# Kernel optimization log

Measured on AMD Instinct MI355X. Metric: run time of the kernel, lower is better.

Reference implementation:

```python
import jax, jax.numpy as jnp
import numpy as np

G = 128          # resolution
NE = 4           # n_emotions
SIGMA = 0.05     # splat kernel width
ETA = 0.01       # global write strength
ALPHA_H = 0.002
ALPHA_E = 0.001
LEAK = 5e-05
RADIUS = max(2, int(3.0 * SIGMA * G / 2.0))   # = 9
W = 2 * RADIUS + 1                            # = 19


def _laplacian(x):
    # 6-neighbor Laplacian with replicate padding; x: [..., G, G, G]
    pad = [(0, 0)] * (x.ndim - 3) + [(1, 1)] * 3
    p = jnp.pad(x, pad, mode='edge')
    c = p[..., 1:-1, 1:-1, 1:-1]
    return (p[..., :-2, 1:-1, 1:-1] + p[..., 2:, 1:-1, 1:-1]
            + p[..., 1:-1, :-2, 1:-1] + p[..., 1:-1, 2:, 1:-1]
            + p[..., 1:-1, 1:-1, :-2] + p[..., 1:-1, 1:-1, 2:]
            - 6.0 * c)


def _splat(H, E, positions, intensities, emotions):
    # Gaussian splat scatter-add into H [G,G,G] and E [NE,G,G,G].
    gp = (positions + 1.0) * 0.5 * (G - 1)                       # [N,3] grid coords
    c = jnp.clip(jnp.floor(gp).astype(jnp.int32), 0, G - 1)      # center cell
    offs = jnp.arange(-RADIUS, RADIUS + 1, dtype=jnp.int32)
    coords = c[:, :, None] + offs[None, None, :]                 # [N,3,W]
    valid = (coords >= 0) & (coords < G)
    cc = jnp.clip(coords, 0, G - 1)
    sig = SIGMA * G / 2.0
    d = coords.astype(gp.dtype) - gp[:, :, None]                 # [N,3,W]
    k1 = jnp.where(valid, jnp.exp(-(d * d) / (2.0 * sig * sig)), 0.0)
    kx, ky, kz = k1[:, 0], k1[:, 1], k1[:, 2]                    # [N,W] each (separable)
    omega = intensities * ETA                                    # [N]
    vals = (omega[:, None, None, None] * kx[:, :, None, None]
            * ky[:, None, :, None] * kz[:, None, None, :])       # [N,W,W,W]
    flat = ((cc[:, 0][:, :, None, None] * G + cc[:, 1][:, None, :, None]) * G
            + cc[:, 2][:, None, None, :]).reshape(-1)            # [N*W^3]
    H_new = H.reshape(-1).at[flat].add(vals.reshape(-1)).reshape(G, G, G)
    E_ch = []
    for e in range(NE):
        ve = (vals * emotions[:, e][:, None, None, None]).reshape(-1)
        E_ch.append(E[e].reshape(-1).at[flat].add(ve).reshape(G, G, G))
    return H_new, jnp.stack(E_ch)


def _step(H, E):
    H2 = jnp.maximum(H * (1.0 - LEAK) + ALPHA_H * _laplacian(H), 0.0)
    E2 = jnp.maximum(E * (1.0 - LEAK) + LEAK + ALPHA_E * _laplacian(E), 0.0)
    return H2, E2


def _sample(H, E, sp):
    # grid_sample trilinear, padding_mode='border', align_corners=True.
    # grid_sample axis convention: sp[...,0]->last axis, sp[...,1]->middle, sp[...,2]->first.
    B, T, _ = sp.shape
    t = jnp.clip((sp.reshape(-1, 3) + 1.0) * 0.5 * (G - 1), 0.0, G - 1)  # [BT,3]
    i0 = jnp.floor(t).astype(jnp.int32)
    f = t - i0
    i0 = jnp.clip(i0, 0, G - 1)
    i1 = jnp.clip(i0 + 1, 0, G - 1)
    x0, y0, z0 = i0[:, 0], i0[:, 1], i0[:, 2]
    x1, y1, z1 = i1[:, 0], i1[:, 1], i1[:, 2]
    fx, fy, fz = f[:, 0], f[:, 1], f[:, 2]

    def interp(vol):  # vol [..., G,G,G] -> [..., BT]
        out = 0.0
        for zi, wz in ((z0, 1.0 - fz), (z1, fz)):
            for yi, wy in ((y0, 1.0 - fy), (y1, fy)):
                for xi, wx in ((x0, 1.0 - fx), (x1, fx)):
                    out = out + vol[..., zi, yi, xi] * (wz * wy * wx)
        return out

    p_H = interp(H).reshape(B, T)
    p_E = interp(E).T.reshape(B, T, NE)
    return p_H, p_E


def setup_inputs() -> dict:
    key = jax.random.key(0)
    k1, k2, k3, k4 = jax.random.split(key, 4)
    N, B, T = 4096, 8, 1024
    return {
        'positions': jax.random.uniform(k1, (N, 3), jnp.float32, -0.95, 0.95),
        'intensities': jax.random.uniform(k2, (N,), jnp.float32),
        'emotions': jax.random.uniform(k3, (N, NE), jnp.float32),
        'sample_positions': jax.random.uniform(k4, (B, T, 3), jnp.float32, -1.0, 1.0),
        'H0': jnp.zeros((G, G, G), jnp.float32),
        'E0': jnp.ones((NE, G, G, G), jnp.float32),
    }


def reference(positions, intensities, emotions, sample_positions, H0, E0):
    H, E = _splat(H0, E0, positions, intensities, emotions)
    H, E = _step(H, E)
    p_H, p_E = _sample(H, E, sample_positions)
    return jnp.concatenate([p_H[..., None], p_E], axis=-1)  # [B,T,1+NE]
```

## Files before the change

### kernel.cpp

```cpp
#include <hip/hip_runtime.h>


namespace {
constexpr int   G      = 128;
constexpr int   G3     = G * G * G;
constexpr int   NE     = 4;
constexpr int   RAD    = 9;
constexpr float SIG    = 0.05f * (float)G * 0.5f;
constexpr float INV2S2 = 1.0f / (2.0f * SIG * SIG);
constexpr float ETA    = 0.01f;
constexpr float A_H    = 0.002f;
constexpr float A_E    = 0.001f;
constexpr float LEAK   = 5e-5f;

constexpr int T0 = 4, T1 = 4, T2 = 32;
constexpr int NT0 = G / T0, NT1 = G / T1, NT2 = G / T2;
constexpr int NTILES = NT0 * NT1 * NT2;
constexpr int CAP = 96;
}

__device__ __forceinline__ int clampi(int v, int lo, int hi) {
    return min(max(v, lo), hi);
}

__global__ void __launch_bounds__(256) bin_meta_kernel(
        const float* __restrict__ pos, const float* __restrict__ inten,
        const float4* __restrict__ emo4,
        int* __restrict__ counts, int* __restrict__ lists,
        float4* __restrict__ meta, int N) {
    const int p    = blockIdx.x * 4 + (threadIdx.x >> 6);
    const int lane = threadIdx.x & 63;
    if (p >= N) return;

    const float gx = (pos[p * 3 + 0] + 1.0f) * 0.5f * (float)(G - 1);
    const float gy = (pos[p * 3 + 1] + 1.0f) * 0.5f * (float)(G - 1);
    const float gz = (pos[p * 3 + 2] + 1.0f) * 0.5f * (float)(G - 1);
    const int c0 = clampi((int)floorf(gx), 0, G - 1);
    const int c1 = clampi((int)floorf(gy), 0, G - 1);
    const int c2 = clampi((int)floorf(gz), 0, G - 1);

    if (lane == 0) {
        meta[2 * p]     = make_float4(gx, gy, gz, inten[p] * ETA);
        meta[2 * p + 1] = emo4[p];
    }

    const int l0 = max(c0 - RAD, 0) >> 2, h0 = min(c0 + RAD, G - 1) >> 2;
    const int l1 = max(c1 - RAD, 0) >> 2, h1 = min(c1 + RAD, G - 1) >> 2;
    const int l2 = max(c2 - RAD, 0) >> 5, h2 = min(c2 + RAD, G - 1) >> 5;
    const int n0 = h0 - l0, n1 = h1 - l1, n2 = h2 - l2;

    for (int s = lane; s < 72; s += 64) {
        const int a = s / 12;
        const int r = s - a * 12;
        const int b = r >> 1;
        const int cs = r & 1;
        if (a <= n0 && b <= n1 && cs <= n2) {
            const int t = ((l0 + a) * NT1 + (l1 + b)) * NT2 + (l2 + cs);
            const int slot = atomicAdd(&counts[t], 1);
            if (slot < CAP) lists[t * CAP + slot] = p;
        }
    }
}

__global__ void __launch_bounds__(256) gather_kernel(
        const float4* __restrict__ meta,
        const float* __restrict__ H0, const float* __restrict__ E0,
        const int* __restrict__ counts, const int* __restrict__ lists,
        float* __restrict__ ws) {
    const int tile = blockIdx.x;
    const int t2 = tile % NT2, t1 = (tile / NT2) % NT1, t0 = tile / (NT2 * NT1);
    const int tid = threadIdx.x;

    __shared__ float kx[CAP * 4];
    __shared__ float ky[CAP * 4];
    __shared__ float kz[CAP * 32];

    const int cnt = min(counts[tile], CAP);
    const int* __restrict__ lst = lists + tile * CAP;

    const int b0 = t0 * T0, b1 = t1 * T1, b2 = t2 * T2;
    for (int t = tid; t < cnt * 40; t += 256) {
        const int n = t / 40;
        const int s = t - n * 40;
        const int p = lst[n];
        const int axis = (s < 4) ? 0 : (s < 8) ? 1 : 2;
        const int off  = (s < 4) ? s : (s < 8) ? s - 4 : s - 8;
        const float4 mg = meta[2 * p];
        const float g = (axis == 0) ? mg.x : (axis == 1) ? mg.y : mg.z;
        const int base = (axis == 0) ? b0 : (axis == 1) ? b1 : b2;
        const int cc = clampi((int)floorf(g), 0, G - 1);
        const int coord = base + off;
        const float d = (float)coord - g;
        float v = (abs(coord - cc) <= RAD) ? __expf(-d * d * INV2S2) : 0.0f;
        if (axis == 0) v *= mg.w;
        if (axis == 0)      kx[n * 4 + off] = v;
        else if (axis == 1) ky[n * 4 + off] = v;
        else                kz[n * 32 + off] = v;
    }
    __syncthreads();

    const int k  = tid & (T2 - 1);
    const int j  = (tid >> 5) & (T1 - 1);
    const int iA = tid >> 7;

    const int x2 = b2 + k, x1 = b1 + j, xA = b0 + iA, xB = xA + 2;
    const int flatA = (xA * G + x1) * G + x2;
    const int flatB = (xB * G + x1) * G + x2;

    float hA = H0[flatA], hB = H0[flatB];
    float eA[NE], eB[NE];
#pragma unroll
    for (int c = 0; c < NE; ++c) {
        eA[c] = E0[c * G3 + flatA];
        eB[c] = E0[c * G3 + flatB];
    }

    for (int n = 0; n < cnt; ++n) {
        const int p = lst[n];
        const float4 mm = meta[2 * p + 1];
        const float kyz = ky[n * 4 + j] * kz[n * 32 + k];
        const float kxA = kx[n * 4 + iA];
        const float kxB = kx[n * 4 + iA + 2];
        const float wA = kxA * kyz;
        const float wB = kxB * kyz;
        hA += wA;            hB += wB;
        eA[0] += wA * mm.x;  eB[0] += wB * mm.x;
        eA[1] += wA * mm.y;  eB[1] += wB * mm.y;
        eA[2] += wA * mm.z;  eB[2] += wB * mm.z;
        eA[3] += wA * mm.w;  eB[3] += wB * mm.w;
    }

    ws[flatA] = hA;  ws[flatB] = hB;
#pragma unroll
    for (int c = 0; c < NE; ++c) {
        ws[(c + 1) * G3 + flatA] = eA[c];
        ws[(c + 1) * G3 + flatB] = eB[c];
    }
}

__device__ __forceinline__ float stepped_at(const float* __restrict__ vol,
                                            int z, int y, int x,
                                            float addc, float alpha) {
    const int zm = max(z - 1, 0), zp = min(z + 1, G - 1);
    const int ym = max(y - 1, 0), yp = min(y + 1, G - 1);
    const int xm = max(x - 1, 0), xp = min(x + 1, G - 1);
    const float cv  = vol[(z * G + y) * G + x];
    const float lap = vol[(zm * G + y) * G + x] + vol[(zp * G + y) * G + x]
                    + vol[(z * G + ym) * G + x] + vol[(z * G + yp) * G + x]
                    + vol[(z * G + y) * G + xm] + vol[(z * G + y) * G + xp]
                    - 6.0f * cv;
    const float s = cv * (1.0f - LEAK) + addc + alpha * lap;
    return fmaxf(s, 0.0f);
}

__global__ void __launch_bounds__(256) sample_kernel(
        const float* __restrict__ sp, const float* __restrict__ ws,
        float* __restrict__ out, int n_out) {
    const int gt = blockIdx.x * blockDim.x + threadIdx.x;
    const int corner = gt & 7;
    const int o = gt >> 3;
    if (o >= n_out) return;
    const int c = o % 5;
    const int p = o / 5;

    const float t0 = fminf(fmaxf((sp[p * 3 + 0] + 1.0f) * 0.5f * (float)(G - 1), 0.0f), (float)(G - 1));
    const float t1 = fminf(fmaxf((sp[p * 3 + 1] + 1.0f) * 0.5f * (float)(G - 1), 0.0f), (float)(G - 1));
    const float t2 = fminf(fmaxf((sp[p * 3 + 2] + 1.0f) * 0.5f * (float)(G - 1), 0.0f), (float)(G - 1));

    const int a0 = (int)floorf(t0);  const float f0 = t0 - (float)a0;
    const int a1 = (int)floorf(t1);  const float f1 = t1 - (float)a1;
    const int a2 = (int)floorf(t2);  const float f2 = t2 - (float)a2;
    const int b0 = min(a0 + 1, G - 1);
    const int b1 = min(a1 + 1, G - 1);
    const int b2 = min(a2 + 1, G - 1);

    const int d0 = corner & 1, d1 = (corner >> 1) & 1, d2 = corner >> 2;
    const int   x = d0 ? b0 : a0;
    const int   y = d1 ? b1 : a1;
    const int   z = d2 ? b2 : a2;
    const float w = (d0 ? f0 : 1.0f - f0) * (d1 ? f1 : 1.0f - f1)
                  * (d2 ? f2 : 1.0f - f2);

    const float* vol  = ws + (size_t)c * G3;
    const float addc  = (c == 0) ? 0.0f : LEAK;
    const float alpha = (c == 0) ? A_H : A_E;

    float v = w * stepped_at(vol, z, y, x, addc, alpha);
    v += __shfl_xor(v, 1);
    v += __shfl_xor(v, 2);
    v += __shfl_xor(v, 4);
    if (corner == 0) out[o] = v;
}

extern "C" void kernel_launch(void* const* d_in, const int* in_sizes, int n_in,
                              void* d_out, int out_size, void* d_ws, size_t ws_size,
                              hipStream_t stream) {
    const float* positions   = (const float*)d_in[0];
    const float* intensities = (const float*)d_in[1];
    const float* emotions    = (const float*)d_in[2];
    const float* sample_pos  = (const float*)d_in[3];
    const float* H0          = (const float*)d_in[4];
    const float* E0          = (const float*)d_in[5];
    float* ws  = (float*)d_ws;
    float* out = (float*)d_out;

    const int N = in_sizes[0] / 3;

    int*    counts = (int*)(ws + 5 * (size_t)G3);
    int*    lists  = counts + NTILES;
    float4* meta   = (float4*)(lists + (size_t)NTILES * CAP);

    hipMemsetAsync(counts, 0, NTILES * sizeof(int), stream);

    bin_meta_kernel<<<(N + 3) / 4, 256, 0, stream>>>(
        positions, intensities, (const float4*)emotions, counts, lists, meta, N);

    gather_kernel<<<NTILES, 256, 0, stream>>>(
        meta, H0, E0, counts, lists, ws);

    const int n_thr = out_size * 8;
    sample_kernel<<<(n_thr + 255) / 256, 256, 0, stream>>>(
        sample_pos, ws, out, out_size);
}
```

Before: 134.2 us.

## Retile gather into 8x4x16 blocks with a packed per-particle LDS table

Changes the binning tile from 4x4x32 to 8x4x16 and moves the gather kernel to 128 threads per block, with each thread accumulating 4 voxels along x instead of 2. Per-particle kernel weights and emotion values go into one packed, stride-32 shared table, so the inner loop reads float4 vectors from LDS instead of reloading the particle index and its emotion values from global memory on every iteration. Per-tile counters are padded to separate cache lines to reduce atomic contention during binning. The cost is a smaller per-tile capacity (88), more tiles per particle, and more registers per thread.

Measured after the change: 137.4 us. 1.02x slower.

```diff
diff --git a/kernel.cpp b/kernel.cpp
--- a/kernel.cpp
+++ b/kernel.cpp
@@ -13,10 +13,12 @@
 constexpr float A_E    = 0.001f;
 constexpr float LEAK   = 5e-5f;
 
-constexpr int T0 = 4, T1 = 4, T2 = 32;
+constexpr int T0 = 8, T1 = 4, T2 = 16;
 constexpr int NT0 = G / T0, NT1 = G / T1, NT2 = G / T2;
 constexpr int NTILES = NT0 * NT1 * NT2;
-constexpr int CAP = 96;
+constexpr int CAP  = 88;
+constexpr int PSTR = 32;
+constexpr int CSTR = 32;
 }
 
 __device__ __forceinline__ int clampi(int v, int lo, int hi) {
@@ -44,97 +46,108 @@
         meta[2 * p + 1] = emo4[p];
     }
 
-    const int l0 = max(c0 - RAD, 0) >> 2, h0 = min(c0 + RAD, G - 1) >> 2;
+    const int l0 = max(c0 - RAD, 0) >> 3, h0 = min(c0 + RAD, G - 1) >> 3;
     const int l1 = max(c1 - RAD, 0) >> 2, h1 = min(c1 + RAD, G - 1) >> 2;
-    const int l2 = max(c2 - RAD, 0) >> 5, h2 = min(c2 + RAD, G - 1) >> 5;
+    const int l2 = max(c2 - RAD, 0) >> 4, h2 = min(c2 + RAD, G - 1) >> 4;
     const int n0 = h0 - l0, n1 = h1 - l1, n2 = h2 - l2;
 
     for (int s = lane; s < 72; s += 64) {
-        const int a = s / 12;
-        const int r = s - a * 12;
-        const int b = r >> 1;
-        const int cs = r & 1;
+        const int a  = s / 18;
+        const int r  = s - a * 18;
+        const int b  = r / 3;
+        const int cs = r - b * 3;
         if (a <= n0 && b <= n1 && cs <= n2) {
             const int t = ((l0 + a) * NT1 + (l1 + b)) * NT2 + (l2 + cs);
-            const int slot = atomicAdd(&counts[t], 1);
+            const int slot = atomicAdd(&counts[t * CSTR], 1);
             if (slot < CAP) lists[t * CAP + slot] = p;
         }
     }
 }
 
-__global__ void __launch_bounds__(256) gather_kernel(
+__global__ void __launch_bounds__(128) gather_kernel(
         const float4* __restrict__ meta,
         const float* __restrict__ H0, const float* __restrict__ E0,
         const int* __restrict__ counts, const int* __restrict__ lists,
         float* __restrict__ ws) {
     const int tile = blockIdx.x;
-    const int t2 = tile % NT2, t1 = (tile / NT2) % NT1, t0 = tile / (NT2 * NT1);
+    const int t2 = tile & (NT2 - 1);
+    const int t1 = (tile >> 3) & (NT1 - 1);
+    const int t0 = tile >> 8;
     const int tid = threadIdx.x;
 
-    __shared__ float kx[CAP * 4];
-    __shared__ float ky[CAP * 4];
-    __shared__ float kz[CAP * 32];
-
-    const int cnt = min(counts[tile], CAP);
+    __shared__ __align__(16) float tab[CAP * PSTR];
+
+    const int cnt = min(counts[tile * CSTR], CAP);
     const int* __restrict__ lst = lists + tile * CAP;
-
     const int b0 = t0 * T0, b1 = t1 * T1, b2 = t2 * T2;
-    for (int t = tid; t < cnt * 40; t += 256) {
-        const int n = t / 40;
-        const int s = t - n * 40;
+
+    for (int t = tid; t < cnt * PSTR; t += 128) {
+        const int n = t >> 5;
+        const int s = t & 31;
         const int p = lst[n];
-        const int axis = (s < 4) ? 0 : (s < 8) ? 1 : 2;
-        const int off  = (s < 4) ? s : (s < 8) ? s - 4 : s - 8;
-        const float4 mg = meta[2 * p];
-        const float g = (axis == 0) ? mg.x : (axis == 1) ? mg.y : mg.z;
-        const int base = (axis == 0) ? b0 : (axis == 1) ? b1 : b2;
-        const int cc = clampi((int)floorf(g), 0, G - 1);
-        const int coord = base + off;
-        const float d = (float)coord - g;
-        float v = (abs(coord - cc) <= RAD) ? __expf(-d * d * INV2S2) : 0.0f;
-        if (axis == 0) v *= mg.w;
-        if (axis == 0)      kx[n * 4 + off] = v;
-        else if (axis == 1) ky[n * 4 + off] = v;
-        else                kz[n * 32 + off] = v;
+        float v;
+        if (s >= 8 && s < 12) {
+            const float4 me = meta[2 * p + 1];
+            const int q = s - 8;
+            v = (q == 0) ? me.x : (q == 1) ? me.y : (q == 2) ? me.z : me.w;
+        } else {
+            const float4 mg = meta[2 * p];
+            float g; int base, off;
+            if (s < 8)       { g = mg.x; base = b0; off = s;      }
+            else if (s < 16) { g = mg.y; base = b1; off = s - 12; }
+            else             { g = mg.z; base = b2; off = s - 16; }
+            const int cc = clampi((int)floorf(g), 0, G - 1);
+            const int coord = base + off;
+            const float d = (float)coord - g;
+            v = (abs(coord - cc) <= RAD) ? __expf(-d * d * INV2S2) : 0.0f;
+            if (s < 8) v *= mg.w;
+        }
+        tab[n * PSTR + s] = v;
     }
     __syncthreads();
 
     const int k  = tid & (T2 - 1);
-    const int j  = (tid >> 5) & (T1 - 1);
-    const int iA = tid >> 7;
-
-    const int x2 = b2 + k, x1 = b1 + j, xA = b0 + iA, xB = xA + 2;
-    const int flatA = (xA * G + x1) * G + x2;
-    const int flatB = (xB * G + x1) * G + x2;
-
-    float hA = H0[flatA], hB = H0[flatB];
-    float eA[NE], eB[NE];
-#pragma unroll
-    for (int c = 0; c < NE; ++c) {
-        eA[c] = E0[c * G3 + flatA];
-        eB[c] = E0[c * G3 + flatB];
-    }
+    const int j  = (tid >> 4) & (T1 - 1);
+    const int i4 = (tid >> 6) * 4;
+
+    const int x2 = b2 + k, x1 = b1 + j;
+    const int flat0 = ((b0 + i4) * G + x1) * G + x2;
+
+    float h[4], e[NE][4];
+#pragma unroll
+    for (int i = 0; i < 4; ++i) {
+        h[i] = H0[flat0 + i * G * G];
+#pragma unroll
+        for (int c = 0; c < NE; ++c) e[c][i] = E0[c * G3 + flat0 + i * G * G];
+    }
+
+    const float* __restrict__ tkx = tab + i4;
+    const float* __restrict__ tky = tab + 12 + j;
+    const float* __restrict__ tkz = tab + 16 + k;
 
     for (int n = 0; n < cnt; ++n) {
-        const int p = lst[n];
-        const float4 mm = meta[2 * p + 1];
-        const float kyz = ky[n * 4 + j] * kz[n * 32 + k];
-        const float kxA = kx[n * 4 + iA];
-        const float kxB = kx[n * 4 + iA + 2];
-        const float wA = kxA * kyz;
-        const float wB = kxB * kyz;
-        hA += wA;            hB += wB;
-        eA[0] += wA * mm.x;  eB[0] += wB * mm.x;
-        eA[1] += wA * mm.y;  eB[1] += wB * mm.y;
-        eA[2] += wA * mm.z;  eB[2] += wB * mm.z;
-        eA[3] += wA * mm.w;  eB[3] += wB * mm.w;
-    }
-
-    ws[flatA] = hA;  ws[flatB] = hB;
-#pragma unroll
-    for (int c = 0; c < NE; ++c) {
-        ws[(c + 1) * G3 + flatA] = eA[c];
-        ws[(c + 1) * G3 + flatB] = eB[c];
+        const float4 kxv = *(const float4*)(tkx + n * PSTR);
+        const float4 emv = *(const float4*)(tab + n * PSTR + 8);
+        const float  kyz = tky[n * PSTR] * tkz[n * PSTR];
+        const float w0 = kxv.x * kyz, w1 = kxv.y * kyz,
+                    w2 = kxv.z * kyz, w3 = kxv.w * kyz;
+        h[0] += w0;  h[1] += w1;  h[2] += w2;  h[3] += w3;
+        e[0][0] += w0 * emv.x; e[0][1] += w1 * emv.x;
+        e[0][2] += w2 * emv.x; e[0][3] += w3 * emv.x;
+        e[1][0] += w0 * emv.y; e[1][1] += w1 * emv.y;
+        e[1][2] += w2 * emv.y; e[1][3] += w3 * emv.y;
+        e[2][0] += w0 * emv.z; e[2][1] += w1 * emv.z;
+        e[2][2] += w2 * emv.z; e[2][3] += w3 * emv.z;
+        e[3][0] += w0 * emv.w; e[3][1] += w1 * emv.w;
+        e[3][2] += w2 * emv.w; e[3][3] += w3 * emv.w;
+    }
+
+#pragma unroll
+    for (int i = 0; i < 4; ++i) {
+        ws[flat0 + i * G * G] = h[i];
+#pragma unroll
+        for (int c = 0; c < NE; ++c)
+            ws[(c + 1) * G3 + flat0 + i * G * G] = e[c][i];
     }
 }
 
@@ -207,15 +220,15 @@
     const int N = in_sizes[0] / 3;
 
     int*    counts = (int*)(ws + 5 * (size_t)G3);
-    int*    lists  = counts + NTILES;
+    int*    lists  = counts + (size_t)NTILES * CSTR;
     float4* meta   = (float4*)(lists + (size_t)NTILES * CAP);
 
-    hipMemsetAsync(counts, 0, NTILES * sizeof(int), stream);
+    hipMemsetAsync(counts, 0, (size_t)NTILES * CSTR * sizeof(int), stream);
 
     bin_meta_kernel<<<(N + 3) / 4, 256, 0, stream>>>(
         positions, intensities, (const float4*)emotions, counts, lists, meta, N);
 
-    gather_kernel<<<NTILES, 256, 0, stream>>>(
+    gather_kernel<<<NTILES, 128, 0, stream>>>(
         meta, H0, E0, counts, lists, ws);
 
     const int n_thr = out_size * 8;
```
